# Kernel tuning notes

Hardware: AMD Instinct MI355X
Metric: run time of the kernel (lower is better)

## Reference

```python
import jax, jax.numpy as jnp
import numpy as np

B, NX, NR, D, H = 8, 512, 512, 256, 256


def setup_inputs() -> dict:
    key = jax.random.key(0)
    ks = jax.random.split(key, 8)
    s = 1.0 / np.sqrt(D)
    sh = 1.0 / np.sqrt(H)
    return {
        "X": jax.random.normal(ks[0], (B, NX, D), dtype=jnp.float32),
        "ref": jax.random.normal(ks[1], (B, NR, D), dtype=jnp.float32),
        "W_X": jax.random.normal(ks[2], (H, D), dtype=jnp.float32) * s,
        "b_X": jax.random.normal(ks[3], (H,), dtype=jnp.float32) * s,
        "W_ref": jax.random.normal(ks[4], (H, D), dtype=jnp.float32) * s,
        "b_ref": jax.random.normal(ks[5], (H,), dtype=jnp.float32) * s,
        "v_w": jax.random.normal(ks[6], (1, H), dtype=jnp.float32) * sh,
        "v_b": jax.random.normal(ks[7], (1,), dtype=jnp.float32) * sh,
    }


def reference(X, ref, W_X, b_X, W_ref, b_ref, v_w, v_b):
    # linear projections: [B, nX, H], [B, nR, H]
    hX = jnp.einsum('bxd,hd->bxh', X, W_X) + b_X
    hR = jnp.einsum('brd,hd->brh', ref, W_ref) + b_ref
    # additive (Bahdanau) scores: [B, nX, nR]
    t = jnp.tanh(hX[:, :, None, :] + hR[:, None, :, :])
    out = jnp.einsum('bxrh,h->bxr', t, v_w[0]) + v_b[0]
    # softmax over the n_X axis (dim=1 in torch)
    attn = jax.nn.softmax(out, axis=1)
    # weighted sum of X per ref position: [B, nR, D]
    weighted_X = jnp.einsum('bxe,bxr->bre', X, attn)
    return weighted_X
```

## Files before the change

kernel.cpp:

```cpp
#include <hip/hip_runtime.h>
#include <math.h>

#define CB 8
#define CNX 512
#define CNR 512
#define CD 256
#define CH 256

__device__ __forceinline__ float fast_rcp(float x) {
#if __has_builtin(__builtin_amdgcn_rcpf)
  return __builtin_amdgcn_rcpf(x);
#else
  return 1.0f / x;
#endif
}
__device__ __forceinline__ float fast_exp2(float x) {
#if __has_builtin(__builtin_amdgcn_exp2f)
  return __builtin_amdgcn_exp2f(x);
#else
  return exp2f(x);
#endif
}

__global__ __launch_bounds__(256) void proj_fused(
    const float* __restrict__ A0, const float* __restrict__ A1,
    const float* __restrict__ W0, const float* __restrict__ W1,
    const float* __restrict__ bias0, const float* __restrict__ bias1,
    float* __restrict__ E0, float* __restrict__ E1) {
  __shared__ float As[16][68];
  __shared__ float Ws[16][68];
  const int K = CD;
  int z = blockIdx.z;
  const float* A = z ? A1 : A0;
  const float* W = z ? W1 : W0;
  const float* bias = z ? bias1 : bias0;
  float* ET = z ? E1 : E0;
  int m0 = blockIdx.x * 64, n0 = blockIdx.y * 64;
  int tid = threadIdx.x;
  int tx = tid & 15, ty = tid >> 4;
  int lrow = tid >> 2, lc4 = tid & 3;
  float acc[4][4] = {};
  const float* pA = A + (size_t)(m0 + lrow) * K + lc4 * 4;
  const float* pW = W + (size_t)(n0 + lrow) * K + lc4 * 4;
  for (int kt = 0; kt < K; kt += 16) {
    float4 av = *(const float4*)(pA + kt);
    float4 wv = *(const float4*)(pW + kt);
    __syncthreads();
    As[lc4 * 4 + 0][lrow] = av.x;
    As[lc4 * 4 + 1][lrow] = av.y;
    As[lc4 * 4 + 2][lrow] = av.z;
    As[lc4 * 4 + 3][lrow] = av.w;
    Ws[lc4 * 4 + 0][lrow] = wv.x;
    Ws[lc4 * 4 + 1][lrow] = wv.y;
    Ws[lc4 * 4 + 2][lrow] = wv.z;
    Ws[lc4 * 4 + 3][lrow] = wv.w;
    __syncthreads();
#pragma unroll
    for (int k = 0; k < 16; k++) {
      float4 a4 = *(const float4*)&As[k][ty * 4];
      float4 w4 = *(const float4*)&Ws[k][tx * 4];
      float am[4] = {a4.x, a4.y, a4.z, a4.w};
      float wm[4] = {w4.x, w4.y, w4.z, w4.w};
#pragma unroll
      for (int i = 0; i < 4; i++)
#pragma unroll
        for (int j = 0; j < 4; j++)
          acc[i][j] = fmaf(am[i], wm[j], acc[i][j]);
    }
  }
  const float K2L = 2.8853900817779268f;
  float4 bv = *(const float4*)(bias + n0 + tx * 4);
  float bm[4] = {bv.x, bv.y, bv.z, bv.w};
  int b = m0 >> 9;
  int xbase = (m0 & 511) + ty * 4;
#pragma unroll
  for (int j = 0; j < 4; j++) {
    int h = n0 + tx * 4 + j;
    float4 o = {fast_exp2(K2L * (acc[0][j] + bm[j])),
                fast_exp2(K2L * (acc[1][j] + bm[j])),
                fast_exp2(K2L * (acc[2][j] + bm[j])),
                fast_exp2(K2L * (acc[3][j] + bm[j]))};
    *(float4*)(ET + ((size_t)b * CH + h) * CNX + xbase) = o;
  }
}

__global__ __launch_bounds__(256) void scores_kernel(
    const float* __restrict__ exT, const float* __restrict__ erT,
    const float* __restrict__ v_w, float* __restrict__ scT) {
  __shared__ float xs[64][32];
  __shared__ float rs[64][32];
  __shared__ float vsh[CH];
  int b = blockIdx.z;
  int x0 = blockIdx.x * 32, r0 = blockIdx.y * 32;
  int tid = threadIdx.x;
  int tx = tid & 15, ty = tid >> 4;
  vsh[tid] = v_w[tid];
  float acc[2][2] = {};
  const float* pX = exT + (size_t)b * CH * CNX + x0;
  const float* pR = erT + (size_t)b * CH * CNR + r0;
  int srow = tid >> 3, sc4 = tid & 7;
  for (int hc = 0; hc < CH; hc += 64) {
    float4 xv0 = *(const float4*)(pX + (size_t)(hc + srow) * CNX + sc4 * 4);
    float4 xv1 = *(const float4*)(pX + (size_t)(hc + srow + 32) * CNX + sc4 * 4);
    float4 rv0 = *(const float4*)(pR + (size_t)(hc + srow) * CNR + sc4 * 4);
    float4 rv1 = *(const float4*)(pR + (size_t)(hc + srow + 32) * CNR + sc4 * 4);
    __syncthreads();
    *(float4*)&xs[srow][sc4 * 4] = xv0;
    *(float4*)&xs[srow + 32][sc4 * 4] = xv1;
    *(float4*)&rs[srow][sc4 * 4] = rv0;
    *(float4*)&rs[srow + 32][sc4 * 4] = rv1;
    __syncthreads();
#pragma unroll 4
    for (int hq = 0; hq < 16; hq++) {
      int h0 = hq * 4;
      float4 vv = *(const float4*)&vsh[hc + h0];
      float2 xa = *(const float2*)&xs[h0 + 0][tx * 2];
      float2 xb = *(const float2*)&xs[h0 + 1][tx * 2];
      float2 xc = *(const float2*)&xs[h0 + 2][tx * 2];
      float2 xd = *(const float2*)&xs[h0 + 3][tx * 2];
      float2 ra = *(const float2*)&rs[h0 + 0][ty * 2];
      float2 rb = *(const float2*)&rs[h0 + 1][ty * 2];
      float2 rc = *(const float2*)&rs[h0 + 2][ty * 2];
      float2 rd = *(const float2*)&rs[h0 + 3][ty * 2];
      float xam[2] = {xa.x, xa.y}, xbm[2] = {xb.x, xb.y};
      float xcm[2] = {xc.x, xc.y}, xdm[2] = {xd.x, xd.y};
      float ram[2] = {ra.x, ra.y}, rbm[2] = {rb.x, rb.y};
      float rcm[2] = {rc.x, rc.y}, rdm[2] = {rd.x, rd.y};
#pragma unroll
      for (int i = 0; i < 2; i++)
#pragma unroll
        for (int j = 0; j < 2; j++) {
          float a = fmaf(ram[i], xam[j], 1.0f);
          float bb = fmaf(rbm[i], xbm[j], 1.0f);
          float c = fmaf(rcm[i], xcm[j], 1.0f);
          float d = fmaf(rdm[i], xdm[j], 1.0f);
          float q12 = a * bb, q34 = c * d;
          float p12 = fmaf(vv.y, a, vv.x * bb);
          float p34 = fmaf(vv.w, c, vv.z * d);
          float num = fmaf(p34, q12, p12 * q34);
          acc[i][j] = fmaf(num, fast_rcp(q12 * q34), acc[i][j]);
        }
    }
  }
  float* pO = scT + ((size_t)b * CNR + r0 + ty * 2) * CNX + x0 + tx * 2;
#pragma unroll
  for (int i = 0; i < 2; i++) {
    float2 o = {-2.0f * acc[i][0], -2.0f * acc[i][1]};
    *(float2*)(pO + (size_t)i * CNX) = o;
  }
}

__global__ __launch_bounds__(256) void wsum_fused(
    const float* __restrict__ scT, const float* __restrict__ X,
    float* __restrict__ out) {
  __shared__ float As[32][33];
  __shared__ float Bs[32][68];
  __shared__ float dn[32];
  const float L2E = 1.4426950408889634f;
  int b = blockIdx.z;
  int r0 = blockIdx.x * 32, d0 = blockIdx.y * 64;
  int tid = threadIdx.x;
  int tx = tid & 15, ty = tid >> 4;
  int arow = tid >> 3, ak4 = tid & 7;
  int brow = tid >> 4, bc4 = tid & 15;
  float acc[2][4] = {};
  float dsum = 0.0f;
  for (int kt = 0; kt < CNX; kt += 32) {
    float4 sv = *(const float4*)(scT + ((size_t)b * CNR + r0 + arow) * CNX + kt + ak4 * 4);
    float4 ev = {fast_exp2(sv.x * L2E), fast_exp2(sv.y * L2E),
                 fast_exp2(sv.z * L2E), fast_exp2(sv.w * L2E)};
    dsum += (ev.x + ev.y) + (ev.z + ev.w);
    float4 bv0 = *(const float4*)(X + ((size_t)b * CNX + kt + brow) * CD + d0 + bc4 * 4);
    float4 bv1 = *(const float4*)(X + ((size_t)b * CNX + kt + brow + 16) * CD + d0 + bc4 * 4);
    __syncthreads();
    As[ak4 * 4 + 0][arow] = ev.x;
    As[ak4 * 4 + 1][arow] = ev.y;
    As[ak4 * 4 + 2][arow] = ev.z;
    As[ak4 * 4 + 3][arow] = ev.w;
    *(float4*)&Bs[brow][bc4 * 4] = bv0;
    *(float4*)&Bs[brow + 16][bc4 * 4] = bv1;
    __syncthreads();
#pragma unroll 8
    for (int k = 0; k < 32; k++) {
      float a0 = As[k][ty * 2], a1 = As[k][ty * 2 + 1];
      float4 b4 = *(const float4*)&Bs[k][tx * 4];
      float bm[4] = {b4.x, b4.y, b4.z, b4.w};
#pragma unroll
      for (int j = 0; j < 4; j++) {
        acc[0][j] = fmaf(a0, bm[j], acc[0][j]);
        acc[1][j] = fmaf(a1, bm[j], acc[1][j]);
      }
    }
  }
  dsum += __shfl_xor(dsum, 1, 64);
  dsum += __shfl_xor(dsum, 2, 64);
  dsum += __shfl_xor(dsum, 4, 64);
  if ((tid & 7) == 0) dn[arow] = dsum;
  __syncthreads();
  float inv0 = fast_rcp(dn[ty * 2]);
  float inv1 = fast_rcp(dn[ty * 2 + 1]);
  float* pO = out + ((size_t)b * CNR + r0 + ty * 2) * CD + d0 + tx * 4;
  float4 o0 = {acc[0][0] * inv0, acc[0][1] * inv0, acc[0][2] * inv0, acc[0][3] * inv0};
  float4 o1 = {acc[1][0] * inv1, acc[1][1] * inv1, acc[1][2] * inv1, acc[1][3] * inv1};
  *(float4*)(pO) = o0;
  *(float4*)(pO + CD) = o1;
}

extern "C" void kernel_launch(void* const* d_in, const int* in_sizes, int n_in,
                              void* d_out, int out_size, void* d_ws, size_t ws_size,
                              hipStream_t stream) {
  const float* X     = (const float*)d_in[0];
  const float* ref   = (const float*)d_in[1];
  const float* W_X   = (const float*)d_in[2];
  const float* b_X   = (const float*)d_in[3];
  const float* W_ref = (const float*)d_in[4];
  const float* b_ref = (const float*)d_in[5];
  const float* v_w   = (const float*)d_in[6];
  float* out = (float*)d_out;
  float* ws  = (float*)d_ws;

  float* exT = ws;
  float* erT = ws + 1048576;
  float* scT = ws + 2097152;

  proj_fused<<<dim3(64, 4, 2), 256, 0, stream>>>(X, ref, W_X, W_ref, b_X, b_ref, exT, erT);
  scores_kernel<<<dim3(16, 16, 8), 256, 0, stream>>>(exT, erT, v_w, scT);
  wsum_fused<<<dim3(16, 4, 8), 256, 0, stream>>>(scT, X, out);
}
```

Measured before the change: 161.1 us.

## Enlarge per-thread tiles to 4x4 and prefetch next tile into registers

The scores and weighted-sum kernels move from 2x2/2x4 per-thread outputs on 32-wide tiles to 4x4 outputs on 64-wide tiles. This raises arithmetic per shared-memory load and halves the number of blocks. All three kernels now load the next K-chunk from global memory into registers while computing the current one, overlapping load latency with math. The trade-off is fewer blocks (512 for scores, 256 for wsum), which lowers occupancy and CU fill on MI355X, plus higher register pressure.

```diff
diff --git a/kernel.cpp b/kernel.cpp
--- a/kernel.cpp
+++ b/kernel.cpp
@@ -42,9 +42,9 @@
   float acc[4][4] = {};
   const float* pA = A + (size_t)(m0 + lrow) * K + lc4 * 4;
   const float* pW = W + (size_t)(n0 + lrow) * K + lc4 * 4;
+  float4 av = *(const float4*)(pA);
+  float4 wv = *(const float4*)(pW);
   for (int kt = 0; kt < K; kt += 16) {
-    float4 av = *(const float4*)(pA + kt);
-    float4 wv = *(const float4*)(pW + kt);
     __syncthreads();
     As[lc4 * 4 + 0][lrow] = av.x;
     As[lc4 * 4 + 1][lrow] = av.y;
@@ -55,6 +55,10 @@
     Ws[lc4 * 4 + 2][lrow] = wv.z;
     Ws[lc4 * 4 + 3][lrow] = wv.w;
     __syncthreads();
+    if (kt + 16 < K) {
+      av = *(const float4*)(pA + kt + 16);
+      wv = *(const float4*)(pW + kt + 16);
+    }
 #pragma unroll
     for (int k = 0; k < 16; k++) {
       float4 a4 = *(const float4*)&As[k][ty * 4];
@@ -84,56 +88,67 @@
   }
 }
 
+#define HCH 32
 __global__ __launch_bounds__(256) void scores_kernel(
     const float* __restrict__ exT, const float* __restrict__ erT,
     const float* __restrict__ v_w, float* __restrict__ scT) {
-  __shared__ float xs[64][32];
-  __shared__ float rs[64][32];
+  __shared__ float xs[HCH][64];
+  __shared__ float rs[HCH][64];
   __shared__ float vsh[CH];
   int b = blockIdx.z;
-  int x0 = blockIdx.x * 32, r0 = blockIdx.y * 32;
+  int x0 = blockIdx.x * 64, r0 = blockIdx.y * 64;
   int tid = threadIdx.x;
   int tx = tid & 15, ty = tid >> 4;
   vsh[tid] = v_w[tid];
-  float acc[2][2] = {};
-  const float* pX = exT + (size_t)b * CH * CNX + x0;
-  const float* pR = erT + (size_t)b * CH * CNR + r0;
-  int srow = tid >> 3, sc4 = tid & 7;
-  for (int hc = 0; hc < CH; hc += 64) {
-    float4 xv0 = *(const float4*)(pX + (size_t)(hc + srow) * CNX + sc4 * 4);
-    float4 xv1 = *(const float4*)(pX + (size_t)(hc + srow + 32) * CNX + sc4 * 4);
-    float4 rv0 = *(const float4*)(pR + (size_t)(hc + srow) * CNR + sc4 * 4);
-    float4 rv1 = *(const float4*)(pR + (size_t)(hc + srow + 32) * CNR + sc4 * 4);
-    __syncthreads();
-    *(float4*)&xs[srow][sc4 * 4] = xv0;
-    *(float4*)&xs[srow + 32][sc4 * 4] = xv1;
-    *(float4*)&rs[srow][sc4 * 4] = rv0;
-    *(float4*)&rs[srow + 32][sc4 * 4] = rv1;
-    __syncthreads();
-#pragma unroll 4
-    for (int hq = 0; hq < 16; hq++) {
+  int sr = ty, sc = tx * 4;
+  const float* pX = exT + (size_t)b * CH * CNX + x0 + sc;
+  const float* pR = erT + (size_t)b * CH * CNR + r0 + sc;
+  float4 xa0 = *(const float4*)(pX + (size_t)sr * CNX);
+  float4 xa1 = *(const float4*)(pX + (size_t)(sr + 16) * CNX);
+  float4 ra0 = *(const float4*)(pR + (size_t)sr * CNR);
+  float4 ra1 = *(const float4*)(pR + (size_t)(sr + 16) * CNR);
+  float acc[4][4] = {};
+  for (int hc = 0; hc < CH; hc += HCH) {
+    __syncthreads();
+    *(float4*)&xs[sr][sc] = xa0;
+    *(float4*)&xs[sr + 16][sc] = xa1;
+    *(float4*)&rs[sr][sc] = ra0;
+    *(float4*)&rs[sr + 16][sc] = ra1;
+    __syncthreads();
+    if (hc + HCH < CH) {
+      xa0 = *(const float4*)(pX + (size_t)(hc + HCH + sr) * CNX);
+      xa1 = *(const float4*)(pX + (size_t)(hc + HCH + sr + 16) * CNX);
+      ra0 = *(const float4*)(pR + (size_t)(hc + HCH + sr) * CNR);
+      ra1 = *(const float4*)(pR + (size_t)(hc + HCH + sr + 16) * CNR);
+    }
+#pragma unroll 2
+    for (int hq = 0; hq < HCH / 4; hq++) {
       int h0 = hq * 4;
       float4 vv = *(const float4*)&vsh[hc + h0];
-      float2 xa = *(const float2*)&xs[h0 + 0][tx * 2];
-      float2 xb = *(const float2*)&xs[h0 + 1][tx * 2];
-      float2 xc = *(const float2*)&xs[h0 + 2][tx * 2];
-      float2 xd = *(const float2*)&xs[h0 + 3][tx * 2];
-      float2 ra = *(const float2*)&rs[h0 + 0][ty * 2];
-      float2 rb = *(const float2*)&rs[h0 + 1][ty * 2];
-      float2 rc = *(const float2*)&rs[h0 + 2][ty * 2];
-      float2 rd = *(const float2*)&rs[h0 + 3][ty * 2];
-      float xam[2] = {xa.x, xa.y}, xbm[2] = {xb.x, xb.y};
-      float xcm[2] = {xc.x, xc.y}, xdm[2] = {xd.x, xd.y};
-      float ram[2] = {ra.x, ra.y}, rbm[2] = {rb.x, rb.y};
-      float rcm[2] = {rc.x, rc.y}, rdm[2] = {rd.x, rd.y};
-#pragma unroll
-      for (int i = 0; i < 2; i++)
-#pragma unroll
-        for (int j = 0; j < 2; j++) {
-          float a = fmaf(ram[i], xam[j], 1.0f);
-          float bb = fmaf(rbm[i], xbm[j], 1.0f);
-          float c = fmaf(rcm[i], xcm[j], 1.0f);
-          float d = fmaf(rdm[i], xdm[j], 1.0f);
+      float4 xv0 = *(const float4*)&xs[h0 + 0][tx * 4];
+      float4 xv1 = *(const float4*)&xs[h0 + 1][tx * 4];
+      float4 xv2 = *(const float4*)&xs[h0 + 2][tx * 4];
+      float4 xv3 = *(const float4*)&xs[h0 + 3][tx * 4];
+      float4 rv0 = *(const float4*)&rs[h0 + 0][ty * 4];
+      float4 rv1 = *(const float4*)&rs[h0 + 1][ty * 4];
+      float4 rv2 = *(const float4*)&rs[h0 + 2][ty * 4];
+      float4 rv3 = *(const float4*)&rs[h0 + 3][ty * 4];
+      float xm0[4] = {xv0.x, xv0.y, xv0.z, xv0.w};
+      float xm1[4] = {xv1.x, xv1.y, xv1.z, xv1.w};
+      float xm2[4] = {xv2.x, xv2.y, xv2.z, xv2.w};
+      float xm3[4] = {xv3.x, xv3.y, xv3.z, xv3.w};
+      float rm0[4] = {rv0.x, rv0.y, rv0.z, rv0.w};
+      float rm1[4] = {rv1.x, rv1.y, rv1.z, rv1.w};
+      float rm2[4] = {rv2.x, rv2.y, rv2.z, rv2.w};
+      float rm3[4] = {rv3.x, rv3.y, rv3.z, rv3.w};
+#pragma unroll
+      for (int i = 0; i < 4; i++)
+#pragma unroll
+        for (int j = 0; j < 4; j++) {
+          float a = fmaf(rm0[i], xm0[j], 1.0f);
+          float bb = fmaf(rm1[i], xm1[j], 1.0f);
+          float c = fmaf(rm2[i], xm2[j], 1.0f);
+          float d = fmaf(rm3[i], xm3[j], 1.0f);
           float q12 = a * bb, q34 = c * d;
           float p12 = fmaf(vv.y, a, vv.x * bb);
           float p34 = fmaf(vv.w, c, vv.z * d);
@@ -142,68 +157,86 @@
         }
     }
   }
-  float* pO = scT + ((size_t)b * CNR + r0 + ty * 2) * CNX + x0 + tx * 2;
-#pragma unroll
-  for (int i = 0; i < 2; i++) {
-    float2 o = {-2.0f * acc[i][0], -2.0f * acc[i][1]};
-    *(float2*)(pO + (size_t)i * CNX) = o;
+  float* pO = scT + ((size_t)b * CNR + r0 + ty * 4) * CNX + x0 + tx * 4;
+#pragma unroll
+  for (int i = 0; i < 4; i++) {
+    float4 o = {-2.0f * acc[i][0], -2.0f * acc[i][1],
+                -2.0f * acc[i][2], -2.0f * acc[i][3]};
+    *(float4*)(pO + (size_t)i * CNX) = o;
   }
 }
 
 __global__ __launch_bounds__(256) void wsum_fused(
     const float* __restrict__ scT, const float* __restrict__ X,
     float* __restrict__ out) {
-  __shared__ float As[32][33];
+  __shared__ float As[32][68];
   __shared__ float Bs[32][68];
-  __shared__ float dn[32];
+  __shared__ float dn[64];
   const float L2E = 1.4426950408889634f;
   int b = blockIdx.z;
-  int r0 = blockIdx.x * 32, d0 = blockIdx.y * 64;
+  int r0 = blockIdx.x * 64, d0 = blockIdx.y * 64;
   int tid = threadIdx.x;
   int tx = tid & 15, ty = tid >> 4;
-  int arow = tid >> 3, ak4 = tid & 7;
-  int brow = tid >> 4, bc4 = tid & 15;
-  float acc[2][4] = {};
+  int ar = tid >> 2, ak = (tid & 3) * 4;
+  int br = tid >> 4, bc = (tid & 15) * 4;
+  const float* pS = scT + ((size_t)b * CNR + r0 + ar) * CNX + ak;
+  const float* pB = X + (size_t)b * CNX * CD + d0 + bc;
+  float acc[4][4] = {};
   float dsum = 0.0f;
+  float4 s0 = *(const float4*)(pS);
+  float4 s1 = *(const float4*)(pS + 16);
+  float4 b0 = *(const float4*)(pB + (size_t)br * CD);
+  float4 b1 = *(const float4*)(pB + (size_t)(br + 16) * CD);
   for (int kt = 0; kt < CNX; kt += 32) {
-    float4 sv = *(const float4*)(scT + ((size_t)b * CNR + r0 + arow) * CNX + kt + ak4 * 4);
-    float4 ev = {fast_exp2(sv.x * L2E), fast_exp2(sv.y * L2E),
-                 fast_exp2(sv.z * L2E), fast_exp2(sv.w * L2E)};
-    dsum += (ev.x + ev.y) + (ev.z + ev.w);
-    float4 bv0 = *(const float4*)(X + ((size_t)b * CNX + kt + brow) * CD + d0 + bc4 * 4);
-    float4 bv1 = *(const float4*)(X + ((size_t)b * CNX + kt + brow + 16) * CD + d0 + bc4 * 4);
-    __syncthreads();
-    As[ak4 * 4 + 0][arow] = ev.x;
-    As[ak4 * 4 + 1][arow] = ev.y;
-    As[ak4 * 4 + 2][arow] = ev.z;
-    As[ak4 * 4 + 3][arow] = ev.w;
-    *(float4*)&Bs[brow][bc4 * 4] = bv0;
-    *(float4*)&Bs[brow + 16][bc4 * 4] = bv1;
-    __syncthreads();
+    float4 e0 = {fast_exp2(s0.x * L2E), fast_exp2(s0.y * L2E),
+                 fast_exp2(s0.z * L2E), fast_exp2(s0.w * L2E)};
+    float4 e1 = {fast_exp2(s1.x * L2E), fast_exp2(s1.y * L2E),
+                 fast_exp2(s1.z * L2E), fast_exp2(s1.w * L2E)};
+    dsum += ((e0.x + e0.y) + (e0.z + e0.w)) + ((e1.x + e1.y) + (e1.z + e1.w));
+    __syncthreads();
+    As[ak + 0][ar] = e0.x;
+    As[ak + 1][ar] = e0.y;
+    As[ak + 2][ar] = e0.z;
+    As[ak + 3][ar] = e0.w;
+    As[ak + 16][ar] = e1.x;
+    As[ak + 17][ar] = e1.y;
+    As[ak + 18][ar] = e1.z;
+    As[ak + 19][ar] = e1.w;
+    *(float4*)&Bs[br][bc] = b0;
+    *(float4*)&Bs[br + 16][bc] = b1;
+    __syncthreads();
+    if (kt + 32 < CNX) {
+      s0 = *(const float4*)(pS + kt + 32);
+      s1 = *(const float4*)(pS + kt + 48);
+      b0 = *(const float4*)(pB + (size_t)(kt + 32 + br) * CD);
+      b1 = *(const float4*)(pB + (size_t)(kt + 32 + br + 16) * CD);
+    }
 #pragma unroll 8
     for (int k = 0; k < 32; k++) {
-      float a0 = As[k][ty * 2], a1 = As[k][ty * 2 + 1];
+      float4 a4 = *(const float4*)&As[k][ty * 4];
       float4 b4 = *(const float4*)&Bs[k][tx * 4];
+      float am[4] = {a4.x, a4.y, a4.z, a4.w};
       float bm[4] = {b4.x, b4.y, b4.z, b4.w};
 #pragma unroll
-      for (int j = 0; j < 4; j++) {
-        acc[0][j] = fmaf(a0, bm[j], acc[0][j]);
-        acc[1][j] = fmaf(a1, bm[j], acc[1][j]);
-      }
+      for (int i = 0; i < 4; i++)
+#pragma unroll
+        for (int j = 0; j < 4; j++)
+          acc[i][j] = fmaf(am[i], bm[j], acc[i][j]);
     }
   }
   dsum += __shfl_xor(dsum, 1, 64);
   dsum += __shfl_xor(dsum, 2, 64);
-  dsum += __shfl_xor(dsum, 4, 64);
-  if ((tid & 7) == 0) dn[arow] = dsum;
+  if ((tid & 3) == 0) dn[ar] = dsum;
   __syncthreads();
-  float inv0 = fast_rcp(dn[ty * 2]);
-  float inv1 = fast_rcp(dn[ty * 2 + 1]);
-  float* pO = out + ((size_t)b * CNR + r0 + ty * 2) * CD + d0 + tx * 4;
-  float4 o0 = {acc[0][0] * inv0, acc[0][1] * inv0, acc[0][2] * inv0, acc[0][3] * inv0};
-  float4 o1 = {acc[1][0] * inv1, acc[1][1] * inv1, acc[1][2] * inv1, acc[1][3] * inv1};
-  *(float4*)(pO) = o0;
-  *(float4*)(pO + CD) = o1;
+  float invm[4] = {fast_rcp(dn[ty * 4 + 0]), fast_rcp(dn[ty * 4 + 1]),
+                   fast_rcp(dn[ty * 4 + 2]), fast_rcp(dn[ty * 4 + 3])};
+  float* pO = out + ((size_t)b * CNR + r0 + ty * 4) * CD + d0 + tx * 4;
+#pragma unroll
+  for (int i = 0; i < 4; i++) {
+    float4 o = {acc[i][0] * invm[i], acc[i][1] * invm[i],
+                acc[i][2] * invm[i], acc[i][3] * invm[i]};
+    *(float4*)(pO + (size_t)i * CD) = o;
+  }
 }
 
 extern "C" void kernel_launch(void* const* d_in, const int* in_sizes, int n_in,
@@ -224,6 +257,6 @@
   float* scT = ws + 2097152;
 
   proj_fused<<<dim3(64, 4, 2), 256, 0, stream>>>(X, ref, W_X, W_ref, b_X, b_ref, exT, erT);
-  scores_kernel<<<dim3(16, 16, 8), 256, 0, stream>>>(exT, erT, v_w, scT);
-  wsum_fused<<<dim3(16, 4, 8), 256, 0, stream>>>(scT, X, out);
-}
+  scores_kernel<<<dim3(8, 8, 8), 256, 0, stream>>>(exT, erT, v_w, scT);
+  wsum_fused<<<dim3(8, 4, 8), 256, 0, stream>>>(scT, X, out);
+}
```

Result: faster. 155.8 us (-3.3%).
